# Optimization experiments

Measured on AMD Instinct MI355X. Metric: run time of the kernel, lower is better.

## Reference

```python
import jax, jax.numpy as jnp
import numpy as np

N_NODES = 50000
N_EDGES = 800000
IN_CH = 128
HID = 128   # 2 * out_channels
OUT = 64
LN_EPS = 1e-5
L2_EPS = 1e-12


def setup_inputs() -> dict:
    key = jax.random.key(0)
    ks = jax.random.split(key, 12)
    x = jax.random.normal(ks[0], (N_NODES, IN_CH), dtype=jnp.float32)
    edge_index = jax.random.randint(ks[1], (2, N_EDGES), 0, N_NODES, dtype=jnp.int64)
    # GCNConv weights (glorot-ish scale) + bias; LayerNorm gamma/beta
    W1 = jax.random.normal(ks[2], (IN_CH, HID), dtype=jnp.float32) * (1.0 / np.sqrt(IN_CH))
    b1 = jnp.zeros((HID,), dtype=jnp.float32)
    g1 = jnp.ones((HID,), dtype=jnp.float32)
    beta1 = jnp.zeros((HID,), dtype=jnp.float32)
    W2 = jax.random.normal(ks[3], (HID, OUT), dtype=jnp.float32) * (1.0 / np.sqrt(HID))
    b2 = jnp.zeros((OUT,), dtype=jnp.float32)
    g2 = jnp.ones((OUT,), dtype=jnp.float32)
    beta2 = jnp.zeros((OUT,), dtype=jnp.float32)
    return {"x": x, "edge_index": edge_index, "W1": W1, "b1": b1, "g1": g1,
            "beta1": beta1, "W2": W2, "b2": b2, "g2": g2, "beta2": beta2}


def _layer_norm(h, gamma, beta):
    mu = jnp.mean(h, axis=-1, keepdims=True)
    var = jnp.mean(jnp.square(h - mu), axis=-1, keepdims=True)
    return (h - mu) * jax.lax.rsqrt(var + LN_EPS) * gamma + beta


def reference(x, edge_index, W1, b1, g1, beta1, W2, b2, g2, beta2):
    # Add self-loops once; compute symmetric GCN normalization (shared by both layers).
    loops = jnp.arange(N_NODES, dtype=edge_index.dtype)
    src = jnp.concatenate([edge_index[0], loops])  # [E+N]
    dst = jnp.concatenate([edge_index[1], loops])  # [E+N]
    deg = jax.ops.segment_sum(jnp.ones_like(dst, dtype=x.dtype), dst,
                              num_segments=N_NODES)
    dinv = jnp.where(deg > 0, jax.lax.rsqrt(deg), 0.0)
    norm = dinv[src] * dinv[dst]  # [E+N]

    def gcn_conv(h, W, b):
        h = h @ W                                   # [N, d_out]
        msg = h[src] * norm[:, None]                # gather + scale  [E+N, d_out]
        agg = jax.ops.segment_sum(msg, dst, num_segments=N_NODES)
        return agg + b

    h = jax.nn.relu(_layer_norm(gcn_conv(x, W1, b1), g1, beta1))
    # Dropout(0.4) is identity in eval mode (correctness baseline).
    h = jax.nn.relu(_layer_norm(gcn_conv(h, W2, b2), g2, beta2))
    nrm = jnp.sqrt(jnp.sum(jnp.square(h), axis=1, keepdims=True))
    return h / jnp.maximum(nrm, L2_EPS)
```

## Files before the change

kernel.cpp:

```cpp
#include <hip/hip_runtime.h>
#include <hip/hip_fp16.h>


#define K_DIM 128

typedef _Float16 f16x8 __attribute__((ext_vector_type(8)));
typedef _Float16 f16x4 __attribute__((ext_vector_type(4)));
typedef float f32x4 __attribute__((ext_vector_type(4)));

__global__ __launch_bounds__(256) void hist_kernel(const int* __restrict__ dst,
                                                   int* counts, int E) {
    int i = blockIdx.x * 256 + threadIdx.x;
    if (i < E) atomicAdd(&counts[dst[i]], 1);
}

__global__ __launch_bounds__(256) void scan_block_kernel(const int* __restrict__ counts,
                                                         int* row_ptr, int* partials,
                                                         float* dinv, int N) {
    __shared__ int sm[256];
    int t = threadIdx.x;
    int i = blockIdx.x * 256 + t;
    int v = (i < N) ? counts[i] : 0;
    if (i < N) dinv[i] = rsqrtf((float)(v + 1));
    sm[t] = v;
    __syncthreads();
    for (int off = 1; off < 256; off <<= 1) {
        int add = (t >= off) ? sm[t - off] : 0;
        __syncthreads();
        sm[t] += add;
        __syncthreads();
    }
    if (i < N) row_ptr[i] = sm[t] - v;
    if (t == 255) partials[blockIdx.x] = sm[255];
}

__global__ __launch_bounds__(256) void scan_partials_kernel(int* partials, int NB) {
    __shared__ int sm[256];
    int t = threadIdx.x;
    int v = (t < NB) ? partials[t] : 0;
    sm[t] = v;
    __syncthreads();
    for (int off = 1; off < 256; off <<= 1) {
        int add = (t >= off) ? sm[t - off] : 0;
        __syncthreads();
        sm[t] += add;
        __syncthreads();
    }
    if (t < NB) partials[t] = sm[t] - v;
}

__global__ __launch_bounds__(256) void fill_kernel(const int* __restrict__ src,
                                                   const int* __restrict__ dst,
                                                   const float* __restrict__ dinv,
                                                   int* row_ptr,
                                                   const int* __restrict__ partials,
                                                   unsigned int* edges, int E) {
    int i = blockIdx.x * 256 + threadIdx.x;
    if (i < E) {
        int d = dst[i];
        int s = src[i];
        int pos = atomicAdd(&row_ptr[d], 1) + partials[d >> 8];
        float w = dinv[s] * dinv[d];
        unsigned int rec = ((unsigned int)__half_as_ushort(__float2half_rn(w)) << 16)
                         | (unsigned int)s;
        edges[pos] = rec;
    }
}

__global__ __launch_bounds__(256) void wt_prep_kernel(const float* __restrict__ W1,
                                                      _Float16* __restrict__ WT) {
    int idx = blockIdx.x * 256 + threadIdx.x;
    if (idx < 128 * 128) {
        int k = idx >> 7, j = idx & 127;
        WT[j * 128 + k] = (_Float16)W1[idx];
    }
}

__global__ __launch_bounds__(256) void gemm1_mfma_kernel(const float* __restrict__ X,
                                                         const _Float16* __restrict__ WT,
                                                         __half* __restrict__ H, int N) {
    __shared__ _Float16 As[64][136];

    int row0 = blockIdx.x * 64;
    {
        int r = threadIdx.x >> 2;
        int c0 = (threadIdx.x & 3) * 32;
        int row = row0 + r;
        if (row < N) {
            const float4* srcp = (const float4*)(X + (size_t)row * 128 + c0);
#pragma unroll
            for (int i = 0; i < 8; ++i) {
                float4 v = srcp[i];
                f16x4 h = {(_Float16)v.x, (_Float16)v.y, (_Float16)v.z, (_Float16)v.w};
                *(f16x4*)&As[r][c0 + 4 * i] = h;
            }
        } else {
            f16x4 z = {};
#pragma unroll
            for (int i = 0; i < 8; ++i) *(f16x4*)&As[r][c0 + 4 * i] = z;
        }
    }
    __syncthreads();

    int wave = threadIdx.x >> 6;
    int lane = threadIdx.x & 63;
    int l15 = lane & 15;
    int k0 = (lane >> 4) * 8;
    int arow = wave * 16 + l15;

    f32x4 acc[8] = {};
#pragma unroll
    for (int ks = 0; ks < 4; ++ks) {
        f16x8 a = *(const f16x8*)&As[arow][ks * 32 + k0];
#pragma unroll
        for (int t = 0; t < 8; ++t) {
            f16x8 b = *(const f16x8*)(WT + (size_t)(t * 16 + l15) * 128 + ks * 32 + k0);
            acc[t] = __builtin_amdgcn_mfma_f32_16x16x32_f16(a, b, acc[t], 0, 0, 0);
        }
    }

    int rbase = row0 + wave * 16 + (lane >> 4) * 4;
#pragma unroll
    for (int t = 0; t < 8; ++t) {
#pragma unroll
        for (int r = 0; r < 4; ++r) {
            int row = rbase + r;
            if (row < N) H[(size_t)row * 128 + t * 16 + l15] = __float2half(acc[t][r]);
        }
    }
}

__global__ __launch_bounds__(256) void gather1_fused_kernel(
    const __half* __restrict__ h1, const float* __restrict__ dinv,
    const int* __restrict__ row_ptr, const int* __restrict__ counts,
    const int* __restrict__ partials, const unsigned int* __restrict__ edges,
    const float* __restrict__ b1, const float* __restrict__ g1,
    const float* __restrict__ beta1, const float* __restrict__ W2,
    __half* __restrict__ h3, int N) {
    __shared__ float lds[4][K_DIM];
    int wave = threadIdx.x >> 6;
    int lane = threadIdx.x & 63;
    int node = blockIdx.x * 4 + wave;
    if (node >= N) return;

    float dd = dinv[node];
    float2 acc = __half22float2(((const __half2*)(h1 + (size_t)node * 128))[lane]);
    acc.x *= dd * dd; acc.y *= dd * dd;

    int end = row_ptr[node] + partials[node >> 8];
    int beg = end - counts[node];
    beg = __builtin_amdgcn_readfirstlane(beg);
    end = __builtin_amdgcn_readfirstlane(end);

    for (int e = beg; e < end; e += 8) {
        unsigned int rec[8];
#pragma unroll
        for (int i = 0; i < 8; ++i) rec[i] = edges[e + i];
        __half2 v[8];
#pragma unroll
        for (int i = 0; i < 8; ++i)
            v[i] = ((const __half2*)(h1 + (size_t)(rec[i] & 0xFFFFu) * 128))[lane];
#pragma unroll
        for (int i = 0; i < 8; ++i) {
            float w = (e + i < end)
                          ? __half2float(__ushort_as_half((unsigned short)(rec[i] >> 16)))
                          : 0.0f;
            float2 f = __half22float2(v[i]);
            acc.x = fmaf(f.x, w, acc.x);
            acc.y = fmaf(f.y, w, acc.y);
        }
    }

    float2 bb = ((const float2*)b1)[lane];
    acc.x += bb.x; acc.y += bb.y;
    float s = acc.x + acc.y;
    for (int off = 32; off; off >>= 1) s += __shfl_xor(s, off);
    float mu = s * (1.0f / 128.0f);
    float dx = acc.x - mu, dy = acc.y - mu;
    float q = dx * dx + dy * dy;
    for (int off = 32; off; off >>= 1) q += __shfl_xor(q, off);
    float rstd = rsqrtf(q * (1.0f / 128.0f) + 1e-5f);
    float2 gg = ((const float2*)g1)[lane];
    float2 be = ((const float2*)beta1)[lane];
    float ox = fmaxf(fmaf(dx * rstd, gg.x, be.x), 0.0f);
    float oy = fmaxf(fmaf(dy * rstd, gg.y, be.y), 0.0f);

    ((float2*)&lds[wave][0])[lane] = make_float2(ox, oy);
    float o = 0.0f;
#pragma unroll 8
    for (int k = 0; k < K_DIM; k += 4) {
        float4 vv = *(const float4*)&lds[wave][k];
        o = fmaf(vv.x, W2[(size_t)(k + 0) * 64 + lane], o);
        o = fmaf(vv.y, W2[(size_t)(k + 1) * 64 + lane], o);
        o = fmaf(vv.z, W2[(size_t)(k + 2) * 64 + lane], o);
        o = fmaf(vv.w, W2[(size_t)(k + 3) * 64 + lane], o);
    }
    h3[(size_t)node * 64 + lane] = __float2half(o);
}

__global__ __launch_bounds__(256) void gather2_fused_kernel(
    const __half* __restrict__ h3, const float* __restrict__ dinv,
    const int* __restrict__ row_ptr, const int* __restrict__ counts,
    const int* __restrict__ partials, const unsigned int* __restrict__ edges,
    const float* __restrict__ b2, const float* __restrict__ g2,
    const float* __restrict__ beta2, float* __restrict__ out, int N) {
    int wave = threadIdx.x >> 6;
    int lane = threadIdx.x & 63;
    int node = blockIdx.x * 4 + wave;
    if (node >= N) return;

    float dd = dinv[node];
    float acc = __half2float(h3[(size_t)node * 64 + lane]) * dd * dd;

    int end = row_ptr[node] + partials[node >> 8];
    int beg = end - counts[node];
    beg = __builtin_amdgcn_readfirstlane(beg);
    end = __builtin_amdgcn_readfirstlane(end);

    for (int e = beg; e < end; e += 8) {
        unsigned int rec[8];
#pragma unroll
        for (int i = 0; i < 8; ++i) rec[i] = edges[e + i];
        __half v[8];
#pragma unroll
        for (int i = 0; i < 8; ++i)
            v[i] = h3[(size_t)(rec[i] & 0xFFFFu) * 64 + lane];
#pragma unroll
        for (int i = 0; i < 8; ++i) {
            float w = (e + i < end)
                          ? __half2float(__ushort_as_half((unsigned short)(rec[i] >> 16)))
                          : 0.0f;
            acc = fmaf(__half2float(v[i]), w, acc);
        }
    }

    float v = acc + b2[lane];
    float s = v;
    for (int off = 32; off; off >>= 1) s += __shfl_xor(s, off);
    float mu = s * (1.0f / 64.0f);
    float d = v - mu;
    float q = d * d;
    for (int off = 32; off; off >>= 1) q += __shfl_xor(q, off);
    float rstd = rsqrtf(q * (1.0f / 64.0f) + 1e-5f);
    float o = fmaxf(fmaf(d * rstd, g2[lane], beta2[lane]), 0.0f);
    float q2 = o * o;
    for (int off = 32; off; off >>= 1) q2 += __shfl_xor(q2, off);
    float nrm = sqrtf(q2);
    out[(size_t)node * 64 + lane] = o / fmaxf(nrm, 1e-12f);
}

extern "C" void kernel_launch(void* const* d_in, const int* in_sizes, int n_in,
                              void* d_out, int out_size, void* d_ws, size_t ws_size,
                              hipStream_t stream) {
    const float* x     = (const float*)d_in[0];
    const int*   ei    = (const int*)d_in[1];
    const float* W1    = (const float*)d_in[2];
    const float* b1    = (const float*)d_in[3];
    const float* g1    = (const float*)d_in[4];
    const float* beta1 = (const float*)d_in[5];
    const float* W2    = (const float*)d_in[6];
    const float* b2    = (const float*)d_in[7];
    const float* g2    = (const float*)d_in[8];
    const float* beta2 = (const float*)d_in[9];

    const int N = in_sizes[0] / 128;
    const int E = in_sizes[1] / 2;
    const int* src = ei;
    const int* dst = ei + E;
    float* out = (float*)d_out;

    char* p = (char*)d_ws;
    auto alloc = [&](size_t bytes) { char* r = p; p += (bytes + 255) & ~(size_t)255; return r; };
    int*          counts   = (int*)alloc((size_t)N * 4);
    int*          row_ptr  = (int*)alloc((size_t)N * 4);
    int*          partials = (int*)alloc(256 * 4);
    float*        dinv     = (float*)alloc((size_t)N * 4);
    unsigned int* edges    = (unsigned int*)alloc(((size_t)E + 64) * 4);
    _Float16*     WT       = (_Float16*)alloc(128 * 128 * 2);
    __half*       h1       = (__half*)alloc((size_t)N * 128 * 2);
    __half*       h3       = (__half*)alloc((size_t)N * 64 * 2);

    const int nb_nodes = (N + 255) / 256;
    const int nb_edges = (E + 255) / 256;
    const int nb_wave_nodes = (N + 3) / 4;

    hipMemsetAsync(counts, 0, (size_t)N * 4, stream);
    hipMemsetAsync(edges + E, 0, 64 * 4, stream);
    hist_kernel<<<nb_edges, 256, 0, stream>>>(dst, counts, E);
    scan_block_kernel<<<nb_nodes, 256, 0, stream>>>(counts, row_ptr, partials, dinv, N);
    scan_partials_kernel<<<1, 256, 0, stream>>>(partials, nb_nodes);
    fill_kernel<<<nb_edges, 256, 0, stream>>>(src, dst, dinv, row_ptr, partials, edges, E);

    wt_prep_kernel<<<64, 256, 0, stream>>>(W1, WT);
    gemm1_mfma_kernel<<<(N + 63) / 64, 256, 0, stream>>>(x, WT, h1, N);

    gather1_fused_kernel<<<nb_wave_nodes, 256, 0, stream>>>(
        h1, dinv, row_ptr, counts, partials, edges, b1, g1, beta1, W2, h3, N);

    gather2_fused_kernel<<<nb_wave_nodes, 256, 0, stream>>>(
        h3, dinv, row_ptr, counts, partials, edges, b2, g2, beta2, out, N);
}
```

Measured before the change: 212.3 us.

## Split wave into sub-groups processing different edges with 8-byte row loads

Both gather kernels now divide each wave into sub-groups (2 in layer one, 4 in layer two). Each sub-group handles a different neighbor edge, and every lane loads four fp16 channels with one 8-byte load instead of one or two channels. Partial sums are merged with cross-lane xor shuffles, and the LayerNorm and L2 reductions are rescaled for the duplicated lanes. The aim is more independent gathers in flight and wider memory transactions per lane. The cost is extra shuffles and reading 16 edge records per iteration, which may read past a row's end.

```diff
diff --git a/kernel.cpp b/kernel.cpp
--- a/kernel.cpp
+++ b/kernel.cpp
@@ -7,6 +7,14 @@
 typedef _Float16 f16x8 __attribute__((ext_vector_type(8)));
 typedef _Float16 f16x4 __attribute__((ext_vector_type(4)));
 typedef float f32x4 __attribute__((ext_vector_type(4)));
+
+__device__ __forceinline__ float2 h2f(unsigned int u) {
+    __half2 h = __builtin_bit_cast(__half2, u);
+    return __half22float2(h);
+}
+__device__ __forceinline__ float wbits(unsigned int r) {
+    return __half2float(__ushort_as_half((unsigned short)(r >> 16)));
+}
 
 __global__ __launch_bounds__(256) void hist_kernel(const int* __restrict__ dst,
                                                    int* counts, int E) {
@@ -142,50 +150,71 @@
     int lane = threadIdx.x & 63;
     int node = blockIdx.x * 4 + wave;
     if (node >= N) return;
-
-    float dd = dinv[node];
-    float2 acc = __half22float2(((const __half2*)(h1 + (size_t)node * 128))[lane]);
-    acc.x *= dd * dd; acc.y *= dd * dd;
+    int sub = lane >> 5;
+    int ch  = lane & 31;
+
+    const uint2* rowp = (const uint2*)h1;
+
+    float4 acc = make_float4(0.0f, 0.0f, 0.0f, 0.0f);
+    if (sub == 0) {
+        float dd = dinv[node];
+        float w = dd * dd;
+        uint2 hv = rowp[(size_t)node * 32 + ch];
+        float2 fa = h2f(hv.x), fb = h2f(hv.y);
+        acc.x = fa.x * w; acc.y = fa.y * w;
+        acc.z = fb.x * w; acc.w = fb.y * w;
+    }
 
     int end = row_ptr[node] + partials[node >> 8];
     int beg = end - counts[node];
     beg = __builtin_amdgcn_readfirstlane(beg);
     end = __builtin_amdgcn_readfirstlane(end);
 
-    for (int e = beg; e < end; e += 8) {
-        unsigned int rec[8];
-#pragma unroll
-        for (int i = 0; i < 8; ++i) rec[i] = edges[e + i];
-        __half2 v[8];
-#pragma unroll
-        for (int i = 0; i < 8; ++i)
-            v[i] = ((const __half2*)(h1 + (size_t)(rec[i] & 0xFFFFu) * 128))[lane];
+    for (int e = beg; e < end; e += 16) {
+        unsigned int rec[16];
+#pragma unroll
+        for (int i = 0; i < 16; ++i) rec[i] = edges[e + i];
+        uint2 v[8];
 #pragma unroll
         for (int i = 0; i < 8; ++i) {
-            float w = (e + i < end)
-                          ? __half2float(__ushort_as_half((unsigned short)(rec[i] >> 16)))
-                          : 0.0f;
-            float2 f = __half22float2(v[i]);
-            acc.x = fmaf(f.x, w, acc.x);
-            acc.y = fmaf(f.y, w, acc.y);
-        }
-    }
-
-    float2 bb = ((const float2*)b1)[lane];
-    acc.x += bb.x; acc.y += bb.y;
-    float s = acc.x + acc.y;
+            unsigned int r = (sub == 0) ? rec[2 * i] : rec[2 * i + 1];
+            v[i] = rowp[(size_t)(r & 0xFFFFu) * 32 + ch];
+        }
+#pragma unroll
+        for (int i = 0; i < 8; ++i) {
+            unsigned int r = (sub == 0) ? rec[2 * i] : rec[2 * i + 1];
+            float w = (e + 2 * i + sub < end) ? wbits(r) : 0.0f;
+            float2 fa = h2f(v[i].x), fb = h2f(v[i].y);
+            acc.x = fmaf(fa.x, w, acc.x);
+            acc.y = fmaf(fa.y, w, acc.y);
+            acc.z = fmaf(fb.x, w, acc.z);
+            acc.w = fmaf(fb.y, w, acc.w);
+        }
+    }
+
+    acc.x += __shfl_xor(acc.x, 32);
+    acc.y += __shfl_xor(acc.y, 32);
+    acc.z += __shfl_xor(acc.z, 32);
+    acc.w += __shfl_xor(acc.w, 32);
+
+    float4 bb = ((const float4*)b1)[ch];
+    acc.x += bb.x; acc.y += bb.y; acc.z += bb.z; acc.w += bb.w;
+    float s = acc.x + acc.y + acc.z + acc.w;
     for (int off = 32; off; off >>= 1) s += __shfl_xor(s, off);
-    float mu = s * (1.0f / 128.0f);
-    float dx = acc.x - mu, dy = acc.y - mu;
-    float q = dx * dx + dy * dy;
+    float mu = s * (1.0f / 256.0f);
+    float d0 = acc.x - mu, d1 = acc.y - mu, d2 = acc.z - mu, d3 = acc.w - mu;
+    float q = d0 * d0 + d1 * d1 + d2 * d2 + d3 * d3;
     for (int off = 32; off; off >>= 1) q += __shfl_xor(q, off);
-    float rstd = rsqrtf(q * (1.0f / 128.0f) + 1e-5f);
-    float2 gg = ((const float2*)g1)[lane];
-    float2 be = ((const float2*)beta1)[lane];
-    float ox = fmaxf(fmaf(dx * rstd, gg.x, be.x), 0.0f);
-    float oy = fmaxf(fmaf(dy * rstd, gg.y, be.y), 0.0f);
-
-    ((float2*)&lds[wave][0])[lane] = make_float2(ox, oy);
+    float rstd = rsqrtf(q * (1.0f / 256.0f) + 1e-5f);
+    float4 gg = ((const float4*)g1)[ch];
+    float4 be = ((const float4*)beta1)[ch];
+    float o0 = fmaxf(fmaf(d0 * rstd, gg.x, be.x), 0.0f);
+    float o1 = fmaxf(fmaf(d1 * rstd, gg.y, be.y), 0.0f);
+    float o2 = fmaxf(fmaf(d2 * rstd, gg.z, be.z), 0.0f);
+    float o3 = fmaxf(fmaf(d3 * rstd, gg.w, be.w), 0.0f);
+
+    if (sub == 0) ((float4*)&lds[wave][0])[ch] = make_float4(o0, o1, o2, o3);
+
     float o = 0.0f;
 #pragma unroll 8
     for (int k = 0; k < K_DIM; k += 4) {
@@ -208,45 +237,87 @@
     int lane = threadIdx.x & 63;
     int node = blockIdx.x * 4 + wave;
     if (node >= N) return;
-
-    float dd = dinv[node];
-    float acc = __half2float(h3[(size_t)node * 64 + lane]) * dd * dd;
+    int sub = lane >> 4;
+    int ch  = lane & 15;
+
+    const uint2* rowp = (const uint2*)h3;
+
+    float4 acc = make_float4(0.0f, 0.0f, 0.0f, 0.0f);
+    if (sub == 0) {
+        float dd = dinv[node];
+        float w = dd * dd;
+        uint2 hv = rowp[(size_t)node * 16 + ch];
+        float2 fa = h2f(hv.x), fb = h2f(hv.y);
+        acc.x = fa.x * w; acc.y = fa.y * w;
+        acc.z = fb.x * w; acc.w = fb.y * w;
+    }
 
     int end = row_ptr[node] + partials[node >> 8];
     int beg = end - counts[node];
     beg = __builtin_amdgcn_readfirstlane(beg);
     end = __builtin_amdgcn_readfirstlane(end);
 
-    for (int e = beg; e < end; e += 8) {
-        unsigned int rec[8];
-#pragma unroll
-        for (int i = 0; i < 8; ++i) rec[i] = edges[e + i];
-        __half v[8];
-#pragma unroll
-        for (int i = 0; i < 8; ++i)
-            v[i] = h3[(size_t)(rec[i] & 0xFFFFu) * 64 + lane];
-#pragma unroll
-        for (int i = 0; i < 8; ++i) {
-            float w = (e + i < end)
-                          ? __half2float(__ushort_as_half((unsigned short)(rec[i] >> 16)))
-                          : 0.0f;
-            acc = fmaf(__half2float(v[i]), w, acc);
-        }
-    }
-
-    float v = acc + b2[lane];
-    float s = v;
+    for (int e = beg; e < end; e += 16) {
+        unsigned int rec[16];
+#pragma unroll
+        for (int i = 0; i < 16; ++i) rec[i] = edges[e + i];
+        uint2 v[4];
+#pragma unroll
+        for (int i = 0; i < 4; ++i) {
+            unsigned int r = (sub == 0) ? rec[4 * i]
+                           : (sub == 1) ? rec[4 * i + 1]
+                           : (sub == 2) ? rec[4 * i + 2]
+                                        : rec[4 * i + 3];
+            v[i] = rowp[(size_t)(r & 0xFFFFu) * 16 + ch];
+        }
+#pragma unroll
+        for (int i = 0; i < 4; ++i) {
+            unsigned int r = (sub == 0) ? rec[4 * i]
+                           : (sub == 1) ? rec[4 * i + 1]
+                           : (sub == 2) ? rec[4 * i + 2]
+                                        : rec[4 * i + 3];
+            float w = (e + 4 * i + sub < end) ? wbits(r) : 0.0f;
+            float2 fa = h2f(v[i].x), fb = h2f(v[i].y);
+            acc.x = fmaf(fa.x, w, acc.x);
+            acc.y = fmaf(fa.y, w, acc.y);
+            acc.z = fmaf(fb.x, w, acc.z);
+            acc.w = fmaf(fb.y, w, acc.w);
+        }
+    }
+
+    acc.x += __shfl_xor(acc.x, 16);
+    acc.y += __shfl_xor(acc.y, 16);
+    acc.z += __shfl_xor(acc.z, 16);
+    acc.w += __shfl_xor(acc.w, 16);
+    acc.x += __shfl_xor(acc.x, 32);
+    acc.y += __shfl_xor(acc.y, 32);
+    acc.z += __shfl_xor(acc.z, 32);
+    acc.w += __shfl_xor(acc.w, 32);
+
+    float4 bb = ((const float4*)b2)[ch];
+    acc.x += bb.x; acc.y += bb.y; acc.z += bb.z; acc.w += bb.w;
+    float s = acc.x + acc.y + acc.z + acc.w;
     for (int off = 32; off; off >>= 1) s += __shfl_xor(s, off);
-    float mu = s * (1.0f / 64.0f);
-    float d = v - mu;
-    float q = d * d;
+    float mu = s * (1.0f / 256.0f);
+    float d0 = acc.x - mu, d1 = acc.y - mu, d2 = acc.z - mu, d3 = acc.w - mu;
+    float q = d0 * d0 + d1 * d1 + d2 * d2 + d3 * d3;
     for (int off = 32; off; off >>= 1) q += __shfl_xor(q, off);
-    float rstd = rsqrtf(q * (1.0f / 64.0f) + 1e-5f);
-    float o = fmaxf(fmaf(d * rstd, g2[lane], beta2[lane]), 0.0f);
-    float q2 = o * o;
+    float rstd = rsqrtf(q * (1.0f / 256.0f) + 1e-5f);
+    float4 gg = ((const float4*)g2)[ch];
+    float4 be = ((const float4*)beta2)[ch];
+    float o0 = fmaxf(fmaf(d0 * rstd, gg.x, be.x), 0.0f);
+    float o1 = fmaxf(fmaf(d1 * rstd, gg.y, be.y), 0.0f);
+    float o2 = fmaxf(fmaf(d2 * rstd, gg.z, be.z), 0.0f);
+    float o3 = fmaxf(fmaf(d3 * rstd, gg.w, be.w), 0.0f);
+
+    float q2 = o0 * o0 + o1 * o1 + o2 * o2 + o3 * o3;
     for (int off = 32; off; off >>= 1) q2 += __shfl_xor(q2, off);
-    float nrm = sqrtf(q2);
-    out[(size_t)node * 64 + lane] = o / fmaxf(nrm, 1e-12f);
+    float nrm = sqrtf(q2) * 0.5f;
+    float inv = 1.0f / fmaxf(nrm, 1e-12f);
+
+    if (sub == 0)
+        ((float4*)(out + (size_t)node * 64))[ch] =
+            make_float4(o0 * inv, o1 * inv, o2 * inv, o3 * inv);
 }
 
 extern "C" void kernel_launch(void* const* d_in, const int* in_sizes, int n_in,
```

New measurement: 269.2 us. 1.27x slower.

## Fuse CSR build stages into one cooperative kernel with grid syncs

Applied to the files above, without the earlier changes.

Replaces two memsets and five small kernels (histogram, block scan, partial scan, fill, weight transpose) with a single cooperative kernel of 512 blocks that uses grid-wide syncs between phases. This removes several kernel launch gaps and the memset launches from the preprocessing chain. In exchange it adds grid barrier costs, runs with a fixed, smaller grid that loops over the data, and leaves the whole GPU waiting at single-block phases such as the partial scan.

```diff
diff --git a/kernel.cpp b/kernel.cpp
--- a/kernel.cpp
+++ b/kernel.cpp
@@ -1,5 +1,8 @@
 #include <hip/hip_runtime.h>
 #include <hip/hip_fp16.h>
+#include <hip/hip_cooperative_groups.h>
+
+namespace cg = cooperative_groups;
 
 
 #define K_DIM 128
@@ -8,71 +11,68 @@
 typedef _Float16 f16x4 __attribute__((ext_vector_type(4)));
 typedef float f32x4 __attribute__((ext_vector_type(4)));
 
-__global__ __launch_bounds__(256) void hist_kernel(const int* __restrict__ dst,
-                                                   int* counts, int E) {
-    int i = blockIdx.x * 256 + threadIdx.x;
-    if (i < E) atomicAdd(&counts[dst[i]], 1);
-}
-
-__global__ __launch_bounds__(256) void scan_block_kernel(const int* __restrict__ counts,
-                                                         int* row_ptr, int* partials,
-                                                         float* dinv, int N) {
+__global__ __launch_bounds__(256) void csr_build_kernel(
+    const int* __restrict__ src, const int* __restrict__ dst,
+    int* counts, int* row_ptr, int* partials, float* dinv,
+    unsigned int* edges, const float* __restrict__ W1, _Float16* WT,
+    int N, int E) {
     __shared__ int sm[256];
-    int t = threadIdx.x;
-    int i = blockIdx.x * 256 + t;
-    int v = (i < N) ? counts[i] : 0;
-    if (i < N) dinv[i] = rsqrtf((float)(v + 1));
-    sm[t] = v;
-    __syncthreads();
-    for (int off = 1; off < 256; off <<= 1) {
-        int add = (t >= off) ? sm[t - off] : 0;
+    cg::grid_group grid = cg::this_grid();
+    const int tid = blockIdx.x * 256 + threadIdx.x;
+    const int nthreads = gridDim.x * 256;
+    const int t = threadIdx.x;
+
+    for (int i = tid; i < N; i += nthreads) counts[i] = 0;
+    if (tid < 64) edges[E + tid] = 0;
+    for (int i = tid; i < 128 * 128; i += nthreads) {
+        int k = i >> 7, j = i & 127;
+        WT[j * 128 + k] = (_Float16)W1[i];
+    }
+    grid.sync();
+
+    for (int i = tid; i < E; i += nthreads) atomicAdd(&counts[dst[i]], 1);
+    grid.sync();
+
+    const int nchunks = (N + 255) / 256;
+    for (int c = blockIdx.x; c < nchunks; c += gridDim.x) {
+        int i = c * 256 + t;
+        int v = (i < N) ? counts[i] : 0;
+        if (i < N) dinv[i] = rsqrtf((float)(v + 1));
+        sm[t] = v;
         __syncthreads();
-        sm[t] += add;
+        for (int off = 1; off < 256; off <<= 1) {
+            int add = (t >= off) ? sm[t - off] : 0;
+            __syncthreads();
+            sm[t] += add;
+            __syncthreads();
+        }
+        if (i < N) row_ptr[i] = sm[t] - v;
+        if (t == 255) partials[c] = sm[255];
         __syncthreads();
     }
-    if (i < N) row_ptr[i] = sm[t] - v;
-    if (t == 255) partials[blockIdx.x] = sm[255];
-}
-
-__global__ __launch_bounds__(256) void scan_partials_kernel(int* partials, int NB) {
-    __shared__ int sm[256];
-    int t = threadIdx.x;
-    int v = (t < NB) ? partials[t] : 0;
-    sm[t] = v;
-    __syncthreads();
-    for (int off = 1; off < 256; off <<= 1) {
-        int add = (t >= off) ? sm[t - off] : 0;
+    grid.sync();
+
+    if (blockIdx.x == 0) {
+        int v = (t < nchunks) ? partials[t] : 0;
+        sm[t] = v;
         __syncthreads();
-        sm[t] += add;
-        __syncthreads();
-    }
-    if (t < NB) partials[t] = sm[t] - v;
-}
-
-__global__ __launch_bounds__(256) void fill_kernel(const int* __restrict__ src,
-                                                   const int* __restrict__ dst,
-                                                   const float* __restrict__ dinv,
-                                                   int* row_ptr,
-                                                   const int* __restrict__ partials,
-                                                   unsigned int* edges, int E) {
-    int i = blockIdx.x * 256 + threadIdx.x;
-    if (i < E) {
+        for (int off = 1; off < 256; off <<= 1) {
+            int add = (t >= off) ? sm[t - off] : 0;
+            __syncthreads();
+            sm[t] += add;
+            __syncthreads();
+        }
+        if (t < nchunks) partials[t] = sm[t] - v;
+    }
+    grid.sync();
+
+    for (int i = tid; i < E; i += nthreads) {
         int d = dst[i];
         int s = src[i];
         int pos = atomicAdd(&row_ptr[d], 1) + partials[d >> 8];
         float w = dinv[s] * dinv[d];
-        unsigned int rec = ((unsigned int)__half_as_ushort(__float2half_rn(w)) << 16)
-                         | (unsigned int)s;
-        edges[pos] = rec;
-    }
-}
-
-__global__ __launch_bounds__(256) void wt_prep_kernel(const float* __restrict__ W1,
-                                                      _Float16* __restrict__ WT) {
-    int idx = blockIdx.x * 256 + threadIdx.x;
-    if (idx < 128 * 128) {
-        int k = idx >> 7, j = idx & 127;
-        WT[j * 128 + k] = (_Float16)W1[idx];
+        edges[pos] = ((unsigned int)__half_as_ushort(__float2half_rn(w)) << 16)
+                   | (unsigned int)s;
     }
 }
 
@@ -280,18 +280,16 @@
     __half*       h1       = (__half*)alloc((size_t)N * 128 * 2);
     __half*       h3       = (__half*)alloc((size_t)N * 64 * 2);
 
-    const int nb_nodes = (N + 255) / 256;
-    const int nb_edges = (E + 255) / 256;
     const int nb_wave_nodes = (N + 3) / 4;
 
-    hipMemsetAsync(counts, 0, (size_t)N * 4, stream);
-    hipMemsetAsync(edges + E, 0, 64 * 4, stream);
-    hist_kernel<<<nb_edges, 256, 0, stream>>>(dst, counts, E);
-    scan_block_kernel<<<nb_nodes, 256, 0, stream>>>(counts, row_ptr, partials, dinv, N);
-    scan_partials_kernel<<<1, 256, 0, stream>>>(partials, nb_nodes);
-    fill_kernel<<<nb_edges, 256, 0, stream>>>(src, dst, dinv, row_ptr, partials, edges, E);
-
-    wt_prep_kernel<<<64, 256, 0, stream>>>(W1, WT);
+    {
+        void* args[] = {(void*)&src, (void*)&dst, (void*)&counts, (void*)&row_ptr,
+                        (void*)&partials, (void*)&dinv, (void*)&edges,
+                        (void*)&W1, (void*)&WT, (void*)&N, (void*)&E};
+        hipLaunchCooperativeKernel((void*)csr_build_kernel, dim3(512), dim3(256),
+                                   args, 0, stream);
+    }
+
     gemm1_mfma_kernel<<<(N + 63) / 64, 256, 0, stream>>>(x, WT, h1, N);
 
     gather1_fused_kernel<<<nb_wave_nodes, 256, 0, stream>>>(
```

Result: slower. 428.3 us (+101.8%).
